# Performance work log

Measured on AMD Instinct MI355X. Metric: run time of the kernel, lower is better.

Reference implementation:

```python
import math
import jax, jax.numpy as jnp
import numpy as np

B, L, N, DM, H = 4, 12, 512, 64, 8
D = DM // H
FACTOR = 5  # args.spatial_factor


def setup_inputs() -> dict:
    key = jax.random.key(0)
    ks = jax.random.split(key, 6)
    s = 1.0 / math.sqrt(DM)
    return {
        "queries": jax.random.normal(ks[0], (B, L, N, DM), jnp.float32),
        "keys": jax.random.normal(ks[1], (B, L, N, DM), jnp.float32),
        "values": jax.random.normal(ks[2], (B, L, N, DM), jnp.float32),
        "Wq": jax.random.normal(ks[3], (DM, DM), jnp.float32) * s,
        "bq": jnp.zeros((DM,), jnp.float32),
        "Wk": jax.random.normal(ks[4], (DM, DM), jnp.float32) * s,
        "bk": jnp.zeros((DM,), jnp.float32),
        "Wv": jax.random.normal(ks[5], (DM, DM), jnp.float32) * s,
        "bv": jnp.zeros((DM,), jnp.float32),
    }


def reference(queries, keys, values, Wq, bq, Wk, bk, Wv, bv):
    # QKV projections (torch nn.Linear), then split heads and move to [B,H,N,L,D]
    q = jnp.transpose((queries @ Wq + bq).reshape(B, L, N, H, D), (0, 3, 2, 1, 4))
    k = jnp.transpose((keys @ Wk + bk).reshape(B, L, N, H, D), (0, 3, 2, 1, 4))
    v = jnp.transpose((values @ Wv + bv).reshape(B, L, N, H, D), (0, 3, 2, 1, 4))

    sample_k = min(FACTOR * int(np.ceil(np.log(N))), N)  # = n_top = effect_N

    # --- _prob_QK: random K sampling over the N (spatial) axis ---
    idx = jax.random.randint(jax.random.key(42), (N, sample_k), 0, N)  # [N, sk]
    K_sample = k[:, :, idx]                       # [B,H,N,sk,L,D] gather
    # Q.unsqueeze(-2) @ K_sample^T -> [B,H,N,L,sk], then transposed to [B,H,L,N,sk]
    qk_s = jnp.einsum('bhnld,bhnsld->bhlns', q, K_sample)
    M = qk_s.max(axis=-1) - qk_s.sum(axis=-1) / N  # sparsity measure [B,H,L,N]
    _, M_top = jax.lax.top_k(M, sample_k)          # [B,H,L,n_top]

    q_t = jnp.transpose(q, (0, 1, 3, 2, 4))        # [B,H,L,N,D]
    Q_red = jnp.take_along_axis(q_t, M_top[..., None], axis=3)  # [B,H,L,n_top,D]
    scores = jnp.einsum('bhltd,bhnld->bhltn', Q_red, k) / math.sqrt(D)

    # --- context: mean of V over nodes, overwritten at top queries ---
    attn = jax.nn.softmax(scores, axis=-1)                        # [B,H,L,n_top,N]
    attn_ret = jnp.einsum('bhltn,bhnld->bhltd', attn, v)          # [B,H,L,n_top,D]
    ctx = jnp.broadcast_to(v.mean(axis=2)[:, :, :, None, :], (B, H, L, N, D))
    bi = jnp.arange(B)[:, None, None, None]
    hi = jnp.arange(H)[None, :, None, None]
    li = jnp.arange(L)[None, None, :, None]
    ctx = ctx.at[bi, hi, li, M_top].set(attn_ret)                 # scatter-write

    out = jnp.transpose(ctx, (0, 2, 3, 1, 4)).reshape(B, L, N, DM)
    return out  # dropout p=0.0 -> identity
```

## Files before the change

### kernel.cpp

```cpp
#include <hip/hip_runtime.h>
#include <stdint.h>
#include <math.h>

#define BB 4
#define LL 12
#define NN 512
#define DMM 64
#define HH 8
#define DD 8
#define SK 35
#define IDX_TOTAL (NN*SK)
#define PADK 12

__device__ __forceinline__ void tf2x32(uint32_t k0, uint32_t k1, uint32_t x0, uint32_t x1,
                                       uint32_t& o0, uint32_t& o1) {
  const uint32_t ks2 = k0 ^ k1 ^ 0x1BD11BDAu;
  uint32_t a = x0 + k0, b = x1 + k1;
#define TF_R(r) { a += b; b = (b << (r)) | (b >> (32 - (r))); b ^= a; }
  TF_R(13) TF_R(15) TF_R(26) TF_R(6)
  a += k1;  b += ks2 + 1u;
  TF_R(17) TF_R(29) TF_R(16) TF_R(24)
  a += ks2; b += k0 + 2u;
  TF_R(13) TF_R(15) TF_R(26) TF_R(6)
  a += k0;  b += k1 + 3u;
  TF_R(17) TF_R(29) TF_R(16) TF_R(24)
  a += k1;  b += ks2 + 4u;
  TF_R(13) TF_R(15) TF_R(26) TF_R(6)
  a += ks2; b += k0 + 5u;
#undef TF_R
  o0 = a; o1 = b;
}

__global__ __launch_bounds__(256) void proj_idx_kernel(
    const float* __restrict__ Xq, const float* __restrict__ Xk, const float* __restrict__ Xv,
    const float* __restrict__ Wq_, const float* __restrict__ Wk_, const float* __restrict__ Wv_,
    const float* __restrict__ bq_, const float* __restrict__ bk_, const float* __restrict__ bv_,
    float* __restrict__ Oq, float* __restrict__ Ok, float* __restrict__ Ov,
    int* __restrict__ idxT) {
  const int tz = blockIdx.y;
  if (tz == 3) {
    int gid = blockIdx.x * 256 + threadIdx.x;
    if (gid < IDX_TOTAL) {
      int r = gid & (NN - 1);
      int s = gid >> 9;
      uint32_t ka, kb;
      tf2x32(0u, 42u, 0u, 1u, ka, kb);
      uint32_t b1, b2;
      tf2x32(ka, kb, 0u, (uint32_t)(r * SK + s), b1, b2);
      idxT[gid] = (int)((b1 ^ b2) & (uint32_t)(NN - 1));
    }
    return;
  }
  const float* X    = (tz == 0) ? Xq  : (tz == 1) ? Xk  : Xv;
  const float* W    = (tz == 0) ? Wq_ : (tz == 1) ? Wk_ : Wv_;
  const float* bias = (tz == 0) ? bq_ : (tz == 1) ? bk_ : bv_;
  float* O          = (tz == 0) ? Oq  : (tz == 1) ? Ok  : Ov;

  __shared__ __align__(16) float Ws[64][64];
  __shared__ __align__(16) float Xs[64][68];
  __shared__ float bs[64];

  const int tid = threadIdx.x;
  const size_t rowBase = (size_t)blockIdx.x * 64;
  const float* Xb = X + rowBase * 64;
  #pragma unroll
  for (int i = 0; i < 4; ++i) {
    int idx = tid + i*256;
    ((float4*)Ws)[idx] = ((const float4*)W)[idx];
    int r = idx >> 4, c = (idx & 15) << 2;
    *(float4*)&Xs[r][c] = ((const float4*)Xb)[idx];
  }
  if (tid < 64) bs[tid] = bias[tid];
  __syncthreads();

  const int hcol = tid & 7;
  const int rb   = tid >> 3;
  float4 bv0 = *(float4*)&bs[hcol*8];
  float4 bv1 = *(float4*)&bs[hcol*8+4];
  float acc[2][8];
  #pragma unroll
  for (int i = 0; i < 2; ++i) {
    acc[i][0]=bv0.x; acc[i][1]=bv0.y; acc[i][2]=bv0.z; acc[i][3]=bv0.w;
    acc[i][4]=bv1.x; acc[i][5]=bv1.y; acc[i][6]=bv1.z; acc[i][7]=bv1.w;
  }
  #pragma unroll 8
  for (int m = 0; m < 64; ++m) {
    float4 w0 = *(const float4*)&Ws[m][hcol*8];
    float4 w1 = *(const float4*)&Ws[m][hcol*8+4];
    float x0 = Xs[rb][m];
    float x1 = Xs[rb+32][m];
    acc[0][0]=fmaf(x0,w0.x,acc[0][0]); acc[0][1]=fmaf(x0,w0.y,acc[0][1]);
    acc[0][2]=fmaf(x0,w0.z,acc[0][2]); acc[0][3]=fmaf(x0,w0.w,acc[0][3]);
    acc[0][4]=fmaf(x0,w1.x,acc[0][4]); acc[0][5]=fmaf(x0,w1.y,acc[0][5]);
    acc[0][6]=fmaf(x0,w1.z,acc[0][6]); acc[0][7]=fmaf(x0,w1.w,acc[0][7]);
    acc[1][0]=fmaf(x1,w0.x,acc[1][0]); acc[1][1]=fmaf(x1,w0.y,acc[1][1]);
    acc[1][2]=fmaf(x1,w0.z,acc[1][2]); acc[1][3]=fmaf(x1,w0.w,acc[1][3]);
    acc[1][4]=fmaf(x1,w1.x,acc[1][4]); acc[1][5]=fmaf(x1,w1.y,acc[1][5]);
    acc[1][6]=fmaf(x1,w1.z,acc[1][6]); acc[1][7]=fmaf(x1,w1.w,acc[1][7]);
  }
  #pragma unroll
  for (int i = 0; i < 2; ++i) {
    size_t R = rowBase + rb + 32*i;
    int bI = (int)(R / (LL*NN));
    int lI = (int)((R / NN) % LL);
    int nI = (int)(R % NN);
    size_t off = ((((size_t)bI*HH + hcol)*LL + lI)*NN + nI)*DD;
    *(float4*)&O[off]     = make_float4(acc[i][0],acc[i][1],acc[i][2],acc[i][3]);
    *(float4*)&O[off + 4] = make_float4(acc[i][4],acc[i][5],acc[i][6],acc[i][7]);
  }
}

__global__ __launch_bounds__(128) void mcomp_kernel(
    const float* __restrict__ Qt, const float* __restrict__ Kt,
    const int* __restrict__ idxT, float* __restrict__ MsW) {
  const int gb = blockIdx.x;
  const int bid = gb >> 2, qtr = gb & 3;
  const int tid = threadIdx.x;
  __shared__ __align__(16) float Ks[NN][PADK];
  const size_t slabOff = (size_t)bid * (NN*DD);

  const float4* kg = (const float4*)(Kt + slabOff);
  #pragma unroll
  for (int i = 0; i < 4; ++i) {
    int r = tid + i*128;
    float4 a = kg[r*2], b = kg[r*2+1];
    *(float4*)&Ks[r][0] = a; *(float4*)&Ks[r][4] = b;
  }
  const int row = qtr*128 + tid;
  const float4* qp = (const float4*)(Qt + slabOff + (size_t)row*DD);
  float4 qa = qp[0], qb = qp[1];
  int jv[SK];
  const int* gi = idxT + row;
  #pragma unroll
  for (int s = 0; s < SK; ++s) jv[s] = gi[s*NN];
  __syncthreads();

  float mx = -INFINITY, sm = 0.f;
  #pragma unroll
  for (int s = 0; s < SK; ++s) {
    int j = jv[s];
    float4 c0 = *(const float4*)&Ks[j][0];
    float4 c1 = *(const float4*)&Ks[j][4];
    float dot = qa.x*c0.x + qa.y*c0.y + qa.z*c0.z + qa.w*c0.w
              + qb.x*c1.x + qb.y*c1.y + qb.z*c1.z + qb.w*c1.w;
    mx = fmaxf(mx, dot);
    sm += dot;
  }
  MsW[bid*NN + row] = mx - sm * (1.0f/NN);
}

__global__ __launch_bounds__(512) void rank_kernel(
    const float* __restrict__ MsW, const float* __restrict__ Vt,
    int* __restrict__ topW, float* __restrict__ vmeanW) {
  const int bid = blockIdx.x;
  const int tid = threadIdx.x;
  const int lane = tid & 63;
  __shared__ uint64_t keys[NN];
  __shared__ __align__(16) float redM[64][8];

  float m = MsW[bid*NN + tid];
  uint32_t u = __float_as_uint(m);
  uint32_t fk = (u & 0x80000000u) ? ~u : (u | 0x80000000u);
  uint64_t my = ((uint64_t)fk << 32) | (uint32_t)(NN - 1 - tid);
  keys[tid] = my;
  __syncthreads();

  int cnt = 0;
  #pragma unroll 16
  for (int j = 0; j < NN; ++j) cnt += (keys[j] > my) ? 1 : 0;
  if (cnt < SK) topW[bid*SK + cnt] = tid;

  if (tid < 64) {
    const size_t slabOff = (size_t)bid * (NN*DD);
    float a[8] = {0,0,0,0,0,0,0,0};
    #pragma unroll
    for (int j = 0; j < 8; ++j) {
      const float4* vp = (const float4*)(Vt + slabOff + (size_t)(lane + 64*j)*DD);
      float4 v0 = vp[0], v1 = vp[1];
      a[0]+=v0.x; a[1]+=v0.y; a[2]+=v0.z; a[3]+=v0.w;
      a[4]+=v1.x; a[5]+=v1.y; a[6]+=v1.z; a[7]+=v1.w;
    }
    *(float4*)&redM[lane][0] = make_float4(a[0],a[1],a[2],a[3]);
    *(float4*)&redM[lane][4] = make_float4(a[4],a[5],a[6],a[7]);
    const int d = lane & 7, g = lane >> 3;
    float s = 0.f;
    #pragma unroll
    for (int k = 0; k < 8; ++k) s += redM[g*8+k][d];
    s += __shfl_xor(s, 8); s += __shfl_xor(s, 16); s += __shfl_xor(s, 32);
    if (lane < 8) vmeanW[bid*8 + lane] = s * (1.0f/NN);
  }
}

__global__ __launch_bounds__(128) void d_kernel(
    const float* __restrict__ Qt, const float* __restrict__ Kt,
    const float* __restrict__ Vt, const int* __restrict__ topW,
    const float* __restrict__ vmeanW, float* __restrict__ out) {
  const int gb = blockIdx.x;
  const int bid = gb >> 2, qtr = gb & 3;
  const int l = bid % LL;
  const int h = (bid / LL) % HH;
  const int b = bid / (LL*HH);
  const int tid = threadIdx.x;
  const int wave = tid >> 6, lane = tid & 63;

  __shared__ int list[SK];
  __shared__ int cnt;
  __shared__ int flagL[128];
  __shared__ __align__(16) float attnOut[128][8];
  __shared__ __align__(16) float redD[2][64][8];
  __shared__ __align__(16) float vm[8];

  const size_t slabOff = (size_t)bid * (NN*DD);

  if (tid == 0) cnt = 0;
  if (tid < 8) vm[tid] = vmeanW[bid*8 + tid];
  flagL[tid] = 0;
  __syncthreads();
  if (tid < SK) {
    int n = topW[bid*SK + tid];
    if ((n >> 7) == qtr) { int s = atomicAdd(&cnt, 1); list[s] = n; }
  }
  __syncthreads();
  const int C = cnt;

  const float4* kp = (const float4*)(Kt + slabOff);
  const float4* vp = (const float4*)(Vt + slabOff);

  for (int it = wave*2; it < C; it += 4) {
    const int n1 = list[it];
    const bool has2 = (it + 1) < C;
    const int n2 = has2 ? list[it+1] : n1;
    const float4* q1p = (const float4*)(Qt + slabOff + (size_t)n1*DD);
    const float4* q2p = (const float4*)(Qt + slabOff + (size_t)n2*DD);
    float4 q1a = q1p[0], q1b = q1p[1];
    float4 q2a = q2p[0], q2b = q2p[1];
    float p1[8], p2[8];
    float mx1 = -INFINITY, mx2 = -INFINITY;
    #pragma unroll
    for (int j = 0; j < 8; ++j) {
      int key = lane + 64*j;
      float4 ca = kp[key*2], cb = kp[key*2+1];
      float s1 = q1a.x*ca.x + q1a.y*ca.y + q1a.z*ca.z + q1a.w*ca.w
               + q1b.x*cb.x + q1b.y*cb.y + q1b.z*cb.z + q1b.w*cb.w;
      float s2 = q2a.x*ca.x + q2a.y*ca.y + q2a.z*ca.z + q2a.w*ca.w
               + q2b.x*cb.x + q2b.y*cb.y + q2b.z*cb.z + q2b.w*cb.w;
      s1 *= 0.35355339059327373f;
      s2 *= 0.35355339059327373f;
      p1[j] = s1; p2[j] = s2;
      mx1 = fmaxf(mx1, s1); mx2 = fmaxf(mx2, s2);
    }
    #pragma unroll
    for (int off = 32; off >= 1; off >>= 1) {
      mx1 = fmaxf(mx1, __shfl_xor(mx1, off));
      mx2 = fmaxf(mx2, __shfl_xor(mx2, off));
    }
    float sum1 = 0.f, sum2 = 0.f;
    #pragma unroll
    for (int j = 0; j < 8; ++j) {
      p1[j] = __expf(p1[j] - mx1); sum1 += p1[j];
      p2[j] = __expf(p2[j] - mx2); sum2 += p2[j];
    }
    #pragma unroll
    for (int off = 32; off >= 1; off >>= 1) {
      sum1 += __shfl_xor(sum1, off);
      sum2 += __shfl_xor(sum2, off);
    }
    float a1[8] = {0,0,0,0,0,0,0,0}, a2[8] = {0,0,0,0,0,0,0,0};
    #pragma unroll
    for (int j = 0; j < 8; ++j) {
      int key = lane + 64*j;
      float4 va = vp[key*2], vb = vp[key*2+1];
      float w1 = p1[j], w2 = p2[j];
      a1[0]=fmaf(w1,va.x,a1[0]); a1[1]=fmaf(w1,va.y,a1[1]);
      a1[2]=fmaf(w1,va.z,a1[2]); a1[3]=fmaf(w1,va.w,a1[3]);
      a1[4]=fmaf(w1,vb.x,a1[4]); a1[5]=fmaf(w1,vb.y,a1[5]);
      a1[6]=fmaf(w1,vb.z,a1[6]); a1[7]=fmaf(w1,vb.w,a1[7]);
      a2[0]=fmaf(w2,va.x,a2[0]); a2[1]=fmaf(w2,va.y,a2[1]);
      a2[2]=fmaf(w2,va.z,a2[2]); a2[3]=fmaf(w2,va.w,a2[3]);
      a2[4]=fmaf(w2,vb.x,a2[4]); a2[5]=fmaf(w2,vb.y,a2[5]);
      a2[6]=fmaf(w2,vb.z,a2[6]); a2[7]=fmaf(w2,vb.w,a2[7]);
    }
    const int d = lane & 7, g = lane >> 3;
    {
      *(float4*)&redD[wave][lane][0] = make_float4(a1[0],a1[1],a1[2],a1[3]);
      *(float4*)&redD[wave][lane][4] = make_float4(a1[4],a1[5],a1[6],a1[7]);
      float s = 0.f;
      #pragma unroll
      for (int k = 0; k < 8; ++k) s += redD[wave][g*8+k][d];
      s += __shfl_xor(s, 8); s += __shfl_xor(s, 16); s += __shfl_xor(s, 32);
      if (lane < 8) attnOut[n1 & 127][lane] = s * (1.0f / sum1);
      if (lane == 0) flagL[n1 & 127] = 1;
    }
    if (has2) {
      *(float4*)&redD[wave][lane][0] = make_float4(a2[0],a2[1],a2[2],a2[3]);
      *(float4*)&redD[wave][lane][4] = make_float4(a2[4],a2[5],a2[6],a2[7]);
      float s = 0.f;
      #pragma unroll
      for (int k = 0; k < 8; ++k) s += redD[wave][g*8+k][d];
      s += __shfl_xor(s, 8); s += __shfl_xor(s, 16); s += __shfl_xor(s, 32);
      if (lane < 8) attnOut[n2 & 127][lane] = s * (1.0f / sum2);
      if (lane == 0) flagL[n2 & 127] = 1;
    }
  }
  __syncthreads();

  {
    float4 o0, o1;
    if (flagL[tid]) { o0 = *(const float4*)&attnOut[tid][0]; o1 = *(const float4*)&attnOut[tid][4]; }
    else            { o0 = *(const float4*)&vm[0];           o1 = *(const float4*)&vm[4]; }
    const int n = qtr*128 + tid;
    float* ob = out + ((size_t)(b*LL + l)*NN + n)*DMM + h*DD;
    *(float4*)&ob[0] = o0;
    *(float4*)&ob[4] = o1;
  }
}

extern "C" void kernel_launch(void* const* d_in, const int* in_sizes, int n_in,
                              void* d_out, int out_size, void* d_ws, size_t ws_size,
                              hipStream_t stream) {
  const float* q  = (const float*)d_in[0];
  const float* k  = (const float*)d_in[1];
  const float* v  = (const float*)d_in[2];
  const float* Wq = (const float*)d_in[3];
  const float* bq = (const float*)d_in[4];
  const float* Wk = (const float*)d_in[5];
  const float* bk = (const float*)d_in[6];
  const float* Wv = (const float*)d_in[7];
  const float* bv = (const float*)d_in[8];
  float* out = (float*)d_out;

  const size_t slab = (size_t)BB*HH*LL*NN*DD;
  float* qT = (float*)d_ws;
  float* kT = qT + slab;
  float* vT = kT + slab;
  int*   idxT = (int*)(vT + slab);
  int*   topW = idxT + IDX_TOTAL;
  float* vmeanW = (float*)(topW + BB*HH*LL*SK);
  float* MsW = vmeanW + BB*HH*LL*8;

  proj_idx_kernel<<<dim3((BB*LL*NN)/64, 4), 256, 0, stream>>>(
      q, k, v, Wq, Wk, Wv, bq, bk, bv, qT, kT, vT, idxT);
  mcomp_kernel<<<BB*HH*LL*4, 128, 0, stream>>>(qT, kT, idxT, MsW);
  rank_kernel<<<BB*HH*LL, 512, 0, stream>>>(MsW, vT, topW, vmeanW);
  d_kernel<<<BB*HH*LL*4, 128, 0, stream>>>(qT, kT, vT, topW, vmeanW, out);
}
```

Baseline: 66.60 us.

## Fuse sparsity measure, top-k ranking and attention into one block-per-slab kernel

Merges the sparsity-measure, rank/top-k and attention kernels into one kernel with one 512-thread block per (b,h,l) slab. Intermediates (M scores, top indices, V mean) now live in shared memory instead of global workspace, and two kernel launches are removed. Wave 0 computes the V mean while waves 1-7 each handle 5 of the 35 top queries. The grid shrinks from 1536 to 384 blocks, which may reduce occupancy and parallelism, and the rank loop now sits directly on the critical path inside each block.

```diff
diff --git a/kernel.cpp b/kernel.cpp
--- a/kernel.cpp
+++ b/kernel.cpp
@@ -110,206 +110,176 @@
   }
 }
 
-__global__ __launch_bounds__(128) void mcomp_kernel(
+__global__ __launch_bounds__(512) void fused_kernel(
     const float* __restrict__ Qt, const float* __restrict__ Kt,
-    const int* __restrict__ idxT, float* __restrict__ MsW) {
-  const int gb = blockIdx.x;
-  const int bid = gb >> 2, qtr = gb & 3;
-  const int tid = threadIdx.x;
-  __shared__ __align__(16) float Ks[NN][PADK];
-  const size_t slabOff = (size_t)bid * (NN*DD);
-
-  const float4* kg = (const float4*)(Kt + slabOff);
-  #pragma unroll
-  for (int i = 0; i < 4; ++i) {
-    int r = tid + i*128;
-    float4 a = kg[r*2], b = kg[r*2+1];
-    *(float4*)&Ks[r][0] = a; *(float4*)&Ks[r][4] = b;
-  }
-  const int row = qtr*128 + tid;
-  const float4* qp = (const float4*)(Qt + slabOff + (size_t)row*DD);
-  float4 qa = qp[0], qb = qp[1];
-  int jv[SK];
-  const int* gi = idxT + row;
-  #pragma unroll
-  for (int s = 0; s < SK; ++s) jv[s] = gi[s*NN];
-  __syncthreads();
-
-  float mx = -INFINITY, sm = 0.f;
-  #pragma unroll
-  for (int s = 0; s < SK; ++s) {
-    int j = jv[s];
-    float4 c0 = *(const float4*)&Ks[j][0];
-    float4 c1 = *(const float4*)&Ks[j][4];
-    float dot = qa.x*c0.x + qa.y*c0.y + qa.z*c0.z + qa.w*c0.w
-              + qb.x*c1.x + qb.y*c1.y + qb.z*c1.z + qb.w*c1.w;
-    mx = fmaxf(mx, dot);
-    sm += dot;
-  }
-  MsW[bid*NN + row] = mx - sm * (1.0f/NN);
-}
-
-__global__ __launch_bounds__(512) void rank_kernel(
-    const float* __restrict__ MsW, const float* __restrict__ Vt,
-    int* __restrict__ topW, float* __restrict__ vmeanW) {
+    const float* __restrict__ Vt, const int* __restrict__ idxT,
+    float* __restrict__ out) {
   const int bid = blockIdx.x;
-  const int tid = threadIdx.x;
-  const int lane = tid & 63;
-  __shared__ uint64_t keys[NN];
-  __shared__ __align__(16) float redM[64][8];
-
-  float m = MsW[bid*NN + tid];
-  uint32_t u = __float_as_uint(m);
-  uint32_t fk = (u & 0x80000000u) ? ~u : (u | 0x80000000u);
-  uint64_t my = ((uint64_t)fk << 32) | (uint32_t)(NN - 1 - tid);
-  keys[tid] = my;
-  __syncthreads();
-
-  int cnt = 0;
-  #pragma unroll 16
-  for (int j = 0; j < NN; ++j) cnt += (keys[j] > my) ? 1 : 0;
-  if (cnt < SK) topW[bid*SK + cnt] = tid;
-
-  if (tid < 64) {
-    const size_t slabOff = (size_t)bid * (NN*DD);
-    float a[8] = {0,0,0,0,0,0,0,0};
-    #pragma unroll
-    for (int j = 0; j < 8; ++j) {
-      const float4* vp = (const float4*)(Vt + slabOff + (size_t)(lane + 64*j)*DD);
-      float4 v0 = vp[0], v1 = vp[1];
-      a[0]+=v0.x; a[1]+=v0.y; a[2]+=v0.z; a[3]+=v0.w;
-      a[4]+=v1.x; a[5]+=v1.y; a[6]+=v1.z; a[7]+=v1.w;
-    }
-    *(float4*)&redM[lane][0] = make_float4(a[0],a[1],a[2],a[3]);
-    *(float4*)&redM[lane][4] = make_float4(a[4],a[5],a[6],a[7]);
-    const int d = lane & 7, g = lane >> 3;
-    float s = 0.f;
-    #pragma unroll
-    for (int k = 0; k < 8; ++k) s += redM[g*8+k][d];
-    s += __shfl_xor(s, 8); s += __shfl_xor(s, 16); s += __shfl_xor(s, 32);
-    if (lane < 8) vmeanW[bid*8 + lane] = s * (1.0f/NN);
-  }
-}
-
-__global__ __launch_bounds__(128) void d_kernel(
-    const float* __restrict__ Qt, const float* __restrict__ Kt,
-    const float* __restrict__ Vt, const int* __restrict__ topW,
-    const float* __restrict__ vmeanW, float* __restrict__ out) {
-  const int gb = blockIdx.x;
-  const int bid = gb >> 2, qtr = gb & 3;
   const int l = bid % LL;
   const int h = (bid / LL) % HH;
   const int b = bid / (LL*HH);
   const int tid = threadIdx.x;
   const int wave = tid >> 6, lane = tid & 63;
 
-  __shared__ int list[SK];
-  __shared__ int cnt;
-  __shared__ int flagL[128];
-  __shared__ __align__(16) float attnOut[128][8];
-  __shared__ __align__(16) float redD[2][64][8];
+  __shared__ __align__(16) float Ks[NN][PADK];
+  __shared__ uint64_t keys[NN];
+  __shared__ int sel[NN];
+  __shared__ int topIdxL[SK + 1];
+  __shared__ __align__(16) float attnOut[SK][8];
+  __shared__ __align__(16) float redD[8][64][8];
   __shared__ __align__(16) float vm[8];
 
   const size_t slabOff = (size_t)bid * (NN*DD);
 
-  if (tid == 0) cnt = 0;
-  if (tid < 8) vm[tid] = vmeanW[bid*8 + tid];
-  flagL[tid] = 0;
-  __syncthreads();
-  if (tid < SK) {
-    int n = topW[bid*SK + tid];
-    if ((n >> 7) == qtr) { int s = atomicAdd(&cnt, 1); list[s] = n; }
-  }
-  __syncthreads();
-  const int C = cnt;
+  {
+    const float4* kg = (const float4*)(Kt + slabOff);
+    float4 a = kg[tid*2], c = kg[tid*2+1];
+    *(float4*)&Ks[tid][0] = a; *(float4*)&Ks[tid][4] = c;
+  }
+  const float4* qp = (const float4*)(Qt + slabOff + (size_t)tid*DD);
+  float4 qa = qp[0], qb = qp[1];
+  int jv[SK];
+  const int* gi = idxT + tid;
+  #pragma unroll
+  for (int s = 0; s < SK; ++s) jv[s] = gi[s*NN];
+  sel[tid] = -1;
+  __syncthreads();
+
+  {
+    float mx = -INFINITY, sm = 0.f;
+    #pragma unroll
+    for (int s = 0; s < SK; ++s) {
+      int j = jv[s];
+      float4 c0 = *(const float4*)&Ks[j][0];
+      float4 c1 = *(const float4*)&Ks[j][4];
+      float dot = qa.x*c0.x + qa.y*c0.y + qa.z*c0.z + qa.w*c0.w
+                + qb.x*c1.x + qb.y*c1.y + qb.z*c1.z + qb.w*c1.w;
+      mx = fmaxf(mx, dot);
+      sm += dot;
+    }
+    float m = mx - sm * (1.0f/NN);
+    uint32_t u = __float_as_uint(m);
+    uint32_t fk = (u & 0x80000000u) ? ~u : (u | 0x80000000u);
+    keys[tid] = ((uint64_t)fk << 32) | (uint32_t)(NN - 1 - tid);
+  }
+  __syncthreads();
+
+  {
+    uint64_t my = keys[tid];
+    int cnt = 0;
+    #pragma unroll 16
+    for (int j = 0; j < NN; ++j) cnt += (keys[j] > my) ? 1 : 0;
+    if (cnt < SK) { topIdxL[cnt] = tid; sel[tid] = cnt; }
+  }
+  __syncthreads();
 
   const float4* kp = (const float4*)(Kt + slabOff);
   const float4* vp = (const float4*)(Vt + slabOff);
 
-  for (int it = wave*2; it < C; it += 4) {
-    const int n1 = list[it];
-    const bool has2 = (it + 1) < C;
-    const int n2 = has2 ? list[it+1] : n1;
-    const float4* q1p = (const float4*)(Qt + slabOff + (size_t)n1*DD);
-    const float4* q2p = (const float4*)(Qt + slabOff + (size_t)n2*DD);
-    float4 q1a = q1p[0], q1b = q1p[1];
-    float4 q2a = q2p[0], q2b = q2p[1];
-    float p1[8], p2[8];
-    float mx1 = -INFINITY, mx2 = -INFINITY;
+  if (wave == 0) {
+    float a[8] = {0,0,0,0,0,0,0,0};
     #pragma unroll
     for (int j = 0; j < 8; ++j) {
-      int key = lane + 64*j;
-      float4 ca = kp[key*2], cb = kp[key*2+1];
-      float s1 = q1a.x*ca.x + q1a.y*ca.y + q1a.z*ca.z + q1a.w*ca.w
-               + q1b.x*cb.x + q1b.y*cb.y + q1b.z*cb.z + q1b.w*cb.w;
-      float s2 = q2a.x*ca.x + q2a.y*ca.y + q2a.z*ca.z + q2a.w*ca.w
-               + q2b.x*cb.x + q2b.y*cb.y + q2b.z*cb.z + q2b.w*cb.w;
-      s1 *= 0.35355339059327373f;
-      s2 *= 0.35355339059327373f;
-      p1[j] = s1; p2[j] = s2;
-      mx1 = fmaxf(mx1, s1); mx2 = fmaxf(mx2, s2);
+      const float4* vr = vp + (size_t)(lane + 64*j)*2;
+      float4 v0 = vr[0], v1 = vr[1];
+      a[0]+=v0.x; a[1]+=v0.y; a[2]+=v0.z; a[3]+=v0.w;
+      a[4]+=v1.x; a[5]+=v1.y; a[6]+=v1.z; a[7]+=v1.w;
     }
+    *(float4*)&redD[0][lane][0] = make_float4(a[0],a[1],a[2],a[3]);
+    *(float4*)&redD[0][lane][4] = make_float4(a[4],a[5],a[6],a[7]);
+    const int d = lane & 7, g = lane >> 3;
+    float s = 0.f;
     #pragma unroll
-    for (int off = 32; off >= 1; off >>= 1) {
-      mx1 = fmaxf(mx1, __shfl_xor(mx1, off));
-      mx2 = fmaxf(mx2, __shfl_xor(mx2, off));
-    }
-    float sum1 = 0.f, sum2 = 0.f;
-    #pragma unroll
-    for (int j = 0; j < 8; ++j) {
-      p1[j] = __expf(p1[j] - mx1); sum1 += p1[j];
-      p2[j] = __expf(p2[j] - mx2); sum2 += p2[j];
-    }
-    #pragma unroll
-    for (int off = 32; off >= 1; off >>= 1) {
-      sum1 += __shfl_xor(sum1, off);
-      sum2 += __shfl_xor(sum2, off);
-    }
-    float a1[8] = {0,0,0,0,0,0,0,0}, a2[8] = {0,0,0,0,0,0,0,0};
-    #pragma unroll
-    for (int j = 0; j < 8; ++j) {
-      int key = lane + 64*j;
-      float4 va = vp[key*2], vb = vp[key*2+1];
-      float w1 = p1[j], w2 = p2[j];
-      a1[0]=fmaf(w1,va.x,a1[0]); a1[1]=fmaf(w1,va.y,a1[1]);
-      a1[2]=fmaf(w1,va.z,a1[2]); a1[3]=fmaf(w1,va.w,a1[3]);
-      a1[4]=fmaf(w1,vb.x,a1[4]); a1[5]=fmaf(w1,vb.y,a1[5]);
-      a1[6]=fmaf(w1,vb.z,a1[6]); a1[7]=fmaf(w1,vb.w,a1[7]);
-      a2[0]=fmaf(w2,va.x,a2[0]); a2[1]=fmaf(w2,va.y,a2[1]);
-      a2[2]=fmaf(w2,va.z,a2[2]); a2[3]=fmaf(w2,va.w,a2[3]);
-      a2[4]=fmaf(w2,vb.x,a2[4]); a2[5]=fmaf(w2,vb.y,a2[5]);
-      a2[6]=fmaf(w2,vb.z,a2[6]); a2[7]=fmaf(w2,vb.w,a2[7]);
-    }
-    const int d = lane & 7, g = lane >> 3;
-    {
-      *(float4*)&redD[wave][lane][0] = make_float4(a1[0],a1[1],a1[2],a1[3]);
-      *(float4*)&redD[wave][lane][4] = make_float4(a1[4],a1[5],a1[6],a1[7]);
-      float s = 0.f;
-      #pragma unroll
-      for (int k = 0; k < 8; ++k) s += redD[wave][g*8+k][d];
-      s += __shfl_xor(s, 8); s += __shfl_xor(s, 16); s += __shfl_xor(s, 32);
-      if (lane < 8) attnOut[n1 & 127][lane] = s * (1.0f / sum1);
-      if (lane == 0) flagL[n1 & 127] = 1;
-    }
-    if (has2) {
-      *(float4*)&redD[wave][lane][0] = make_float4(a2[0],a2[1],a2[2],a2[3]);
-      *(float4*)&redD[wave][lane][4] = make_float4(a2[4],a2[5],a2[6],a2[7]);
-      float s = 0.f;
-      #pragma unroll
-      for (int k = 0; k < 8; ++k) s += redD[wave][g*8+k][d];
-      s += __shfl_xor(s, 8); s += __shfl_xor(s, 16); s += __shfl_xor(s, 32);
-      if (lane < 8) attnOut[n2 & 127][lane] = s * (1.0f / sum2);
-      if (lane == 0) flagL[n2 & 127] = 1;
-    }
+    for (int k = 0; k < 8; ++k) s += redD[0][g*8+k][d];
+    s += __shfl_xor(s, 8); s += __shfl_xor(s, 16); s += __shfl_xor(s, 32);
+    if (lane < 8) vm[lane] = s * (1.0f/NN);
+  } else {
+    const int base = (wave - 1) * 5;
+    auto do_rows = [&](int t1, int t2, bool has2) {
+      const int n1 = topIdxL[t1];
+      const int n2 = has2 ? topIdxL[t2] : n1;
+      const float4* q1p = (const float4*)(Qt + slabOff + (size_t)n1*DD);
+      const float4* q2p = (const float4*)(Qt + slabOff + (size_t)n2*DD);
+      float4 q1a = q1p[0], q1b = q1p[1];
+      float4 q2a = q2p[0], q2b = q2p[1];
+      float p1[8], p2[8];
+      float mx1 = -INFINITY, mx2 = -INFINITY;
+      #pragma unroll
+      for (int j = 0; j < 8; ++j) {
+        int key = lane + 64*j;
+        float4 ca = kp[key*2], cb = kp[key*2+1];
+        float s1 = q1a.x*ca.x + q1a.y*ca.y + q1a.z*ca.z + q1a.w*ca.w
+                 + q1b.x*cb.x + q1b.y*cb.y + q1b.z*cb.z + q1b.w*cb.w;
+        float s2 = q2a.x*ca.x + q2a.y*ca.y + q2a.z*ca.z + q2a.w*ca.w
+                 + q2b.x*cb.x + q2b.y*cb.y + q2b.z*cb.z + q2b.w*cb.w;
+        s1 *= 0.35355339059327373f;
+        s2 *= 0.35355339059327373f;
+        p1[j] = s1; p2[j] = s2;
+        mx1 = fmaxf(mx1, s1); mx2 = fmaxf(mx2, s2);
+      }
+      #pragma unroll
+      for (int off = 32; off >= 1; off >>= 1) {
+        mx1 = fmaxf(mx1, __shfl_xor(mx1, off));
+        mx2 = fmaxf(mx2, __shfl_xor(mx2, off));
+      }
+      float sum1 = 0.f, sum2 = 0.f;
+      #pragma unroll
+      for (int j = 0; j < 8; ++j) {
+        p1[j] = __expf(p1[j] - mx1); sum1 += p1[j];
+        p2[j] = __expf(p2[j] - mx2); sum2 += p2[j];
+      }
+      #pragma unroll
+      for (int off = 32; off >= 1; off >>= 1) {
+        sum1 += __shfl_xor(sum1, off);
+        sum2 += __shfl_xor(sum2, off);
+      }
+      float a1[8] = {0,0,0,0,0,0,0,0}, a2[8] = {0,0,0,0,0,0,0,0};
+      #pragma unroll
+      for (int j = 0; j < 8; ++j) {
+        int key = lane + 64*j;
+        float4 va = vp[key*2], vb = vp[key*2+1];
+        float w1 = p1[j], w2 = p2[j];
+        a1[0]=fmaf(w1,va.x,a1[0]); a1[1]=fmaf(w1,va.y,a1[1]);
+        a1[2]=fmaf(w1,va.z,a1[2]); a1[3]=fmaf(w1,va.w,a1[3]);
+        a1[4]=fmaf(w1,vb.x,a1[4]); a1[5]=fmaf(w1,vb.y,a1[5]);
+        a1[6]=fmaf(w1,vb.z,a1[6]); a1[7]=fmaf(w1,vb.w,a1[7]);
+        a2[0]=fmaf(w2,va.x,a2[0]); a2[1]=fmaf(w2,va.y,a2[1]);
+        a2[2]=fmaf(w2,va.z,a2[2]); a2[3]=fmaf(w2,va.w,a2[3]);
+        a2[4]=fmaf(w2,vb.x,a2[4]); a2[5]=fmaf(w2,vb.y,a2[5]);
+        a2[6]=fmaf(w2,vb.z,a2[6]); a2[7]=fmaf(w2,vb.w,a2[7]);
+      }
+      const int d = lane & 7, g = lane >> 3;
+      {
+        *(float4*)&redD[wave][lane][0] = make_float4(a1[0],a1[1],a1[2],a1[3]);
+        *(float4*)&redD[wave][lane][4] = make_float4(a1[4],a1[5],a1[6],a1[7]);
+        float s = 0.f;
+        #pragma unroll
+        for (int k = 0; k < 8; ++k) s += redD[wave][g*8+k][d];
+        s += __shfl_xor(s, 8); s += __shfl_xor(s, 16); s += __shfl_xor(s, 32);
+        if (lane < 8) attnOut[t1][lane] = s * (1.0f / sum1);
+      }
+      if (has2) {
+        *(float4*)&redD[wave][lane][0] = make_float4(a2[0],a2[1],a2[2],a2[3]);
+        *(float4*)&redD[wave][lane][4] = make_float4(a2[4],a2[5],a2[6],a2[7]);
+        float s = 0.f;
+        #pragma unroll
+        for (int k = 0; k < 8; ++k) s += redD[wave][g*8+k][d];
+        s += __shfl_xor(s, 8); s += __shfl_xor(s, 16); s += __shfl_xor(s, 32);
+        if (lane < 8) attnOut[t2][lane] = s * (1.0f / sum2);
+      }
+    };
+    do_rows(base, base + 1, true);
+    do_rows(base + 2, base + 3, true);
+    do_rows(base + 4, base + 4, false);
   }
   __syncthreads();
 
   {
+    int t = sel[tid];
     float4 o0, o1;
-    if (flagL[tid]) { o0 = *(const float4*)&attnOut[tid][0]; o1 = *(const float4*)&attnOut[tid][4]; }
-    else            { o0 = *(const float4*)&vm[0];           o1 = *(const float4*)&vm[4]; }
-    const int n = qtr*128 + tid;
-    float* ob = out + ((size_t)(b*LL + l)*NN + n)*DMM + h*DD;
+    if (t >= 0) { o0 = *(const float4*)&attnOut[t][0]; o1 = *(const float4*)&attnOut[t][4]; }
+    else        { o0 = *(const float4*)&vm[0];         o1 = *(const float4*)&vm[4]; }
+    float* ob = out + ((size_t)(b*LL + l)*NN + tid)*DMM + h*DD;
     *(float4*)&ob[0] = o0;
     *(float4*)&ob[4] = o1;
   }
@@ -334,13 +304,8 @@
   float* kT = qT + slab;
   float* vT = kT + slab;
   int*   idxT = (int*)(vT + slab);
-  int*   topW = idxT + IDX_TOTAL;
-  float* vmeanW = (float*)(topW + BB*HH*LL*SK);
-  float* MsW = vmeanW + BB*HH*LL*8;
 
   proj_idx_kernel<<<dim3((BB*LL*NN)/64, 4), 256, 0, stream>>>(
       q, k, v, Wq, Wk, Wv, bq, bk, bv, qT, kT, vT, idxT);
-  mcomp_kernel<<<BB*HH*LL*4, 128, 0, stream>>>(qT, kT, idxT, MsW);
-  rank_kernel<<<BB*HH*LL, 512, 0, stream>>>(MsW, vT, topW, vmeanW);
-  d_kernel<<<BB*HH*LL*4, 128, 0, stream>>>(qT, kT, vT, topW, vmeanW, out);
+  fused_kernel<<<BB*HH*LL, 512, 0, stream>>>(qT, kT, vT, idxT, out);
 }
```

New measurement: 59.94 us. -10.0%, faster.
